# Optimization experiments

Hardware: AMD Instinct MI355X
Metric: run time of the kernel (lower is better)

The kernel has to match this reference:

```python
import jax, jax.numpy as jnp
import numpy as np

N = 2800        # real node count (before hardcoded pad)
NPAD = 3000     # module pads node dim to 3000
F_IN = 8192     # node_features
H1 = 256        # dim_h1 (GCLSTM in_channels)
H2 = 128        # GCLSTM out_channels
E = 179200      # edges (avg degree 64)


def setup_inputs() -> dict:
    key = jax.random.key(0)
    ks = jax.random.split(key, 12)
    inp = {
        "x": jax.random.normal(ks[0], (N, F_IN), jnp.float32),
        "edge_index": jax.random.randint(ks[1], (2, E), 0, N, dtype=jnp.int64),
        "edge_weight": jax.random.uniform(ks[2], (E,), jnp.float32),
        "h0": jax.random.normal(ks[3], (NPAD, H2), jnp.float32),
        "c0": jax.random.normal(ks[4], (NPAD, H2), jnp.float32),
        # fc0: node_features -> dim_h1
        "fc0_w": jax.random.normal(ks[5], (F_IN, H1), jnp.float32) / np.float32(np.sqrt(F_IN)),
        "fc0_b": jnp.zeros((H1,), jnp.float32),
        # GCLSTM gate params, stacked over gates [i, f, c, o]
        "Wx": jax.random.normal(ks[6], (4, H1, H2), jnp.float32) / np.float32(np.sqrt(H1)),
        "bg": jnp.zeros((4, H2), jnp.float32),
        # ChebConv (K=2) weights per gate: theta_0, theta_1, bias
        "cw0": jax.random.normal(ks[7], (4, H2, H2), jnp.float32) / np.float32(np.sqrt(H2)),
        "cw1": jax.random.normal(ks[8], (4, H2, H2), jnp.float32) / np.float32(np.sqrt(H2)),
        "cb": jnp.zeros((4, H2), jnp.float32),
        # final fc: 128 -> 1
        "fc_w": jax.random.normal(ks[9], (H2, 1), jnp.float32) / np.float32(np.sqrt(H2)),
        "fc_b": jnp.zeros((1,), jnp.float32),
    }
    return inp


def _cheb_scaled_laplacian(edge_index, edge_weight, num_nodes):
    # ChebConv 'sym' norm with lambda_max=2: L_hat = -D^{-1/2} A D^{-1/2}
    # (diagonal of scaled Laplacian cancels to zero with fill_value=-1 self loops)
    row, col = edge_index[0], edge_index[1]
    deg = jax.ops.segment_sum(edge_weight, row, num_segments=num_nodes)
    dinv = jnp.where(deg > 0, jax.lax.rsqrt(jnp.where(deg > 0, deg, 1.0)), 0.0)
    return -dinv[row] * edge_weight * dinv[col]  # per-edge weight of L_hat


def reference(x, edge_weight, h0, c0, fc0_w, fc0_b, Wx, bg, cw0, cw1, cb,
              fc_w, fc_b, edge_index):
    n_real = x.shape[0]
    # hardcoded zero-padding of node dim to 3000
    xp = jnp.concatenate([x, jnp.zeros((NPAD - n_real, x.shape[1]), x.dtype)], axis=0)
    z = jax.nn.relu(xp @ fc0_w + fc0_b)                       # [3000, 256]

    row, col = edge_index[0], edge_index[1]
    w_hat = _cheb_scaled_laplacian(edge_index, edge_weight, NPAD)
    # Chebyshev T1 term: L_hat @ H  (shared across all four gates)
    T1 = jax.ops.segment_sum(w_hat[:, None] * h0[row], col, num_segments=NPAD)  # [3000,128]

    # all four gate pre-activations at once: X W_x + ChebConv(H) + b
    gates = (jnp.einsum('nf,gfo->gno', z, Wx)
             + jnp.einsum('nd,gdo->gno', h0, cw0)
             + jnp.einsum('nd,gdo->gno', T1, cw1)
             + (bg + cb)[:, None, :])                          # [4, 3000, 128]

    i = jax.nn.sigmoid(gates[0])
    f = jax.nn.sigmoid(gates[1])
    t = jnp.tanh(gates[2])
    o = jax.nn.sigmoid(gates[3])
    c_new = f * c0 + i * t
    h_new = o * jnp.tanh(c_new)                                # [3000, 128]

    out = (jax.nn.relu(h_new) @ fc_w + fc_b)[:, 0]             # squeeze last dim
    out = out[:n_real]                                         # drop padding rows
    return out, h_new
```

## Files before the change

### kernel.cpp

```cpp
#include <hip/hip_runtime.h>
#include <math.h>

#define N_REAL 2800
#define NPAD   3000
#define F_IN   8192
#define H1     256
#define H2     128
#define NE     179200
#define UDIM   512
#define NGATE  512
#define MPAD   3072
#define SPLITK 8
#define KCH    (F_IN / SPLITK)
#define NHB    64
#define EPB    (NE / NHB)

typedef _Float16 half8_t __attribute__((ext_vector_type(8)));
typedef _Float16 half4_t __attribute__((ext_vector_type(4)));
typedef float    floatx4 __attribute__((ext_vector_type(4)));

__device__ __forceinline__ void async_g2l_16(const _Float16* g, _Float16* l) {
    __builtin_amdgcn_global_load_lds(
        (const __attribute__((address_space(1))) unsigned int*)g,
        (__attribute__((address_space(3))) unsigned int*)l, 16, 0, 0);
}

__global__ __launch_bounds__(256)
void prep_kernel(const float* __restrict__ w, const float* __restrict__ Wx,
                 const float* __restrict__ cw0, const float* __restrict__ cw1,
                 const float* __restrict__ bg, const float* __restrict__ cb,
                 const float* __restrict__ h0, const int* __restrict__ ei,
                 const float* __restrict__ ew,
                 _Float16* __restrict__ wTp, _Float16* __restrict__ Wcp,
                 float* __restrict__ biasv, _Float16* __restrict__ U16,
                 float* __restrict__ deg, int* __restrict__ counts,
                 int* __restrict__ cnt_pT) {
    __shared__ __align__(16) char pmem[24576];
    int b = blockIdx.x;
    int t = threadIdx.x;
    if (b < NHB) {
        float* sdeg = (float*)pmem;
        int*   scnt = (int*)(pmem + 12288);
        for (int i = t; i < 3072; i += 256) { sdeg[i] = 0.f; scnt[i] = 0; }
        __syncthreads();
        int e0 = b * EPB;
        for (int i = t; i < EPB; i += 256) {
            int e = e0 + i;
            atomicAdd(&sdeg[ei[e]], ew[e]);
            atomicAdd(&scnt[ei[NE + e]], 1);
        }
        __syncthreads();
        for (int i = t; i < 3072; i += 256) {
            atomicAdd(&deg[i], sdeg[i]);
            atomicAdd(&counts[i], scnt[i]);
            cnt_pT[i * NHB + b] = scnt[i];
        }
    } else if (b < 2112) {
        float (*tile)[33] = (float(*)[33])pmem;
        int bb = b - NHB;
        int k0 = (bb & 255) * 32;
        int n0 = (bb >> 8) * 32;
        int tx = t & 31, ty = t >> 5;
#pragma unroll
        for (int r = 0; r < 4; r++)
            tile[ty + r * 8][tx] = w[(size_t)(k0 + ty + r * 8) * H1 + n0 + tx];
        __syncthreads();
        if (t < 128) {
            int u_l = t >> 5;
            int n_l = t & 31;
            half8_t h;
#pragma unroll
            for (int j = 0; j < 8; j++) h[j] = (_Float16)tile[u_l * 8 + j][n_l];
            *(half8_t*)&wTp[(((size_t)(k0 >> 3) + u_l) * H1 + n0 + n_l) * 8] = h;
        }
    } else if (b < 3136) {
        int idx = (b - 2112) * 256 + t;
        if (idx < UDIM * NGATE) {
            int col = idx >> 9;
            int f   = idx & 511;
            int g = col >> 7, o = col & 127;
            float v;
            if (f < H1)            v = Wx[((size_t)g * H1 + f) * H2 + o];
            else if (f < H1 + H2)  v = cw0[((size_t)g * H2 + (f - H1)) * H2 + o];
            else                   v = cw1[((size_t)g * H2 + (f - H1 - H2)) * H2 + o];
            Wcp[(((size_t)(f >> 3)) * NGATE + col) * 8 + (f & 7)] = (_Float16)v;
            if (f == 0) biasv[col] = bg[col] + cb[col];
        }
    } else {
        int q = (b - 3136) * 256 + t;
        int m = q >> 5;
        int o4 = (q & 31) * 4;
        half4_t h = {};
        if (m < NPAD) {
            float4 v = *(const float4*)&h0[(size_t)m * H2 + o4];
            h[0] = (_Float16)v.x; h[1] = (_Float16)v.y; h[2] = (_Float16)v.z; h[3] = (_Float16)v.w;
        }
        *(half4_t*)&U16[(size_t)m * UDIM + H1 + o4] = h;
    }
}

__device__ __forceinline__ void stage_b1(const _Float16* __restrict__ wTp,
                                         _Float16 (*bs)[256][8], int wave, int lane, size_t kb8) {
    const _Float16* bbase = wTp + kb8 * (H1 * 8);
#pragma unroll
    for (int q = 0; q < 2; q++) {
        int u = wave * 2 + q;
#pragma unroll
        for (int rg = 0; rg < 4; rg++)
            async_g2l_16(bbase + ((size_t)u * H1 + rg * 64 + lane) * 8,
                         &bs[u][rg * 64 + lane][0]);
    }
}

__device__ __forceinline__ void put_a1(_Float16 (*as)[64][8], int arow, int aseg,
                                       const float4* A) {
    half8_t hlo, hhi;
    hlo[0] = (_Float16)A[0].x; hlo[1] = (_Float16)A[0].y; hlo[2] = (_Float16)A[0].z; hlo[3] = (_Float16)A[0].w;
    hlo[4] = (_Float16)A[1].x; hlo[5] = (_Float16)A[1].y; hlo[6] = (_Float16)A[1].z; hlo[7] = (_Float16)A[1].w;
    hhi[0] = (_Float16)A[2].x; hhi[1] = (_Float16)A[2].y; hhi[2] = (_Float16)A[2].z; hhi[3] = (_Float16)A[2].w;
    hhi[4] = (_Float16)A[3].x; hhi[5] = (_Float16)A[3].y; hhi[6] = (_Float16)A[3].z; hhi[7] = (_Float16)A[3].w;
    *(half8_t*)&as[aseg * 2][arow][0]     = hlo;
    *(half8_t*)&as[aseg * 2 + 1][arow][0] = hhi;
}

__device__ __forceinline__ void comp64(floatx4 (&acc)[4][4], _Float16 (*as)[64][8],
                                       _Float16 (*bs)[256][8], int wave, int u4, int l16) {
#pragma unroll
    for (int ks = 0; ks < 2; ks++) {
        half8_t a[4], bfr[4];
#pragma unroll
        for (int i = 0; i < 4; i++) a[i] = *(const half8_t*)&as[ks * 4 + u4][i * 16 + l16][0];
#pragma unroll
        for (int j = 0; j < 4; j++) bfr[j] = *(const half8_t*)&bs[ks * 4 + u4][wave * 64 + j * 16 + l16][0];
#pragma unroll
        for (int i = 0; i < 4; i++)
#pragma unroll
            for (int j = 0; j < 4; j++)
                acc[i][j] = __builtin_amdgcn_mfma_f32_16x16x32_f16(a[i], bfr[j], acc[i][j], 0, 0, 0);
    }
}

#define LOADA1(A, off) do { if (avalid) { \
    A[0] = *(const float4*)(agp + (off));      A[1] = *(const float4*)(agp + (off) + 4); \
    A[2] = *(const float4*)(agp + (off) + 8);  A[3] = *(const float4*)(agp + (off) + 12); } } while (0)

__global__ __launch_bounds__(256, 2)
void gemm1_fused(const float* __restrict__ x, const _Float16* __restrict__ wTp,
                 float* __restrict__ P) {
    __shared__ __align__(16) _Float16 As[2][8][64][8];
    __shared__ __align__(16) _Float16 Bs[2][8][256][8];
    const int t = threadIdx.x;
    const int wave = t >> 6, lane = t & 63;
    const int l16 = lane & 15, u4 = lane >> 4;
    const int m0 = blockIdx.x * 64;
    const int kbase = blockIdx.y * KCH;

    const int arow = t >> 2;
    const int aseg = t & 3;
    const bool avalid = (m0 + arow) < N_REAL;
    const float* agp = x + (size_t)(m0 + arow) * F_IN + kbase + aseg * 16;

    floatx4 acc[4][4] = {};
    float4 A0[4] = {}, A1[4] = {};

    LOADA1(A0, 0);
    stage_b1(wTp, Bs[0], wave, lane, (size_t)kbase >> 3);
    put_a1(As[0], arow, aseg, A0);
    LOADA1(A1, 64);
    LOADA1(A0, 128);
    __syncthreads();

    for (int q8 = 0; q8 < 8; ++q8) {
        const int k = 2 * q8;
        stage_b1(wTp, Bs[1], wave, lane, (size_t)(kbase + (k + 1) * 64) >> 3);
        put_a1(As[1], arow, aseg, A1);
        if (q8 < 7) LOADA1(A1, (k + 3) * 64);
        comp64(acc, As[0], Bs[0], wave, u4, l16);
        __syncthreads();
        if (q8 < 7) {
            stage_b1(wTp, Bs[0], wave, lane, (size_t)(kbase + (k + 2) * 64) >> 3);
            put_a1(As[0], arow, aseg, A0);
            if (q8 < 6) LOADA1(A0, (k + 4) * 64);
        }
        comp64(acc, As[1], Bs[1], wave, u4, l16);
        __syncthreads();
    }

    float* Pb = P + ((size_t)blockIdx.y * MPAD + m0) * H1;
#pragma unroll
    for (int i = 0; i < 4; i++)
#pragma unroll
        for (int j = 0; j < 4; j++) {
            int n = wave * 64 + j * 16 + l16;
#pragma unroll
            for (int r = 0; r < 4; r++)
                Pb[(size_t)(i * 16 + u4 * 4 + r) * H1 + n] = acc[i][j][r];
        }
}

__device__ __forceinline__ void zreduce_body(int zb, int t, const float* __restrict__ P,
                                             const float* __restrict__ fc0_b,
                                             _Float16* __restrict__ U16) {
    int q = zb * 256 + t;
    int m = q >> 6;
    int n4 = (q & 63) * 4;
    float s0 = 0.f, s1 = 0.f, s2 = 0.f, s3 = 0.f;
#pragma unroll
    for (int sk = 0; sk < SPLITK; sk++) {
        float4 p = *(const float4*)&P[((size_t)sk * MPAD + m) * H1 + n4];
        s0 += p.x; s1 += p.y; s2 += p.z; s3 += p.w;
    }
    float4 bb = *(const float4*)&fc0_b[n4];
    half4_t h;
    h[0] = (_Float16)fmaxf(s0 + bb.x, 0.f);
    h[1] = (_Float16)fmaxf(s1 + bb.y, 0.f);
    h[2] = (_Float16)fmaxf(s2 + bb.z, 0.f);
    h[3] = (_Float16)fmaxf(s3 + bb.w, 0.f);
    *(half4_t*)&U16[(size_t)m * UDIM + n4] = h;
}

__global__ __launch_bounds__(256)
void scatterz_kernel(const int* __restrict__ ei, const int* __restrict__ counts,
                     const float* __restrict__ deg, const int* __restrict__ cnt_pT,
                     int* __restrict__ offsets, float* __restrict__ dinv,
                     int* __restrict__ eid,
                     const float* __restrict__ P, const float* __restrict__ fc0_b,
                     _Float16* __restrict__ U16) {
    __shared__ int sb[3072];
    __shared__ int wt[4];
    int b = blockIdx.x;
    int t = threadIdx.x;
    if (b < NHB + 1) {
        int i0 = t * 12;
        int v[12]; int s = 0;
#pragma unroll
        for (int j = 0; j < 12; j++) { v[j] = counts[i0 + j]; s += v[j]; }
        int incl = s;
#pragma unroll
        for (int d = 1; d < 64; d <<= 1) {
            int n = __shfl_up(incl, d);
            if ((t & 63) >= d) incl += n;
        }
        if ((t & 63) == 63) wt[t >> 6] = incl;
        __syncthreads();
        int wbase = 0;
#pragma unroll
        for (int w = 0; w < 4; w++) wbase += (w < (t >> 6)) ? wt[w] : 0;
        int run = wbase + incl - s;
        if (b < NHB) {
#pragma unroll
            for (int j = 0; j < 12; j++) {
                const int4* cp = (const int4*)(cnt_pT + (size_t)(i0 + j) * NHB);
                int base = 0;
#pragma unroll
                for (int q4 = 0; q4 < 16; q4++) {
                    int4 v4 = cp[q4];
                    int i4 = q4 * 4;
                    base += (i4     < b ? v4.x : 0) + (i4 + 1 < b ? v4.y : 0)
                          + (i4 + 2 < b ? v4.z : 0) + (i4 + 3 < b ? v4.w : 0);
                }
                sb[i0 + j] = run + base;
                run += v[j];
            }
            __syncthreads();
            int e0 = b * EPB;
            for (int i = t; i < EPB; i += 256) {
                int e = e0 + i;
                int c = ei[NE + e];
                int p = atomicAdd(&sb[c], 1);
                eid[p] = e;
            }
        } else {
#pragma unroll
            for (int j = 0; j < 12; j++) { offsets[i0 + j] = run; run += v[j]; }
            for (int i = t; i < NPAD; i += 256) {
                float d = deg[i];
                dinv[i] = (d > 0.f) ? rsqrtf(d) : 0.f;
            }
        }
    } else {
        zreduce_body(b - NHB - 1, t, P, fc0_b, U16);
    }
}

__global__ __launch_bounds__(128)
void gather_kernel(const int* __restrict__ ei, const float* __restrict__ ew,
                   const float* __restrict__ h0, const float* __restrict__ dinv,
                   const int* __restrict__ offsets, const int* __restrict__ eid,
                   _Float16* __restrict__ U16) {
    __shared__ int   sr[128];
    __shared__ float sw[128];
    int n = blockIdx.x;
    int t = threadIdx.x;
    int beg = offsets[n], end = offsets[n + 1];
    float dc = dinv[n];
    float acc = 0.f;
    for (int base = beg; base < end; base += 128) {
        int j = base + t;
        if (j < end) {
            int e = eid[j];
            int r = ei[e];
            sr[t] = r;
            sw[t] = -dinv[r] * ew[e];
        }
        __syncthreads();
        int cnt = min(128, end - base);
        int k = 0;
        for (; k + 8 <= cnt; k += 8) {
            int   r0 = sr[k],   r1 = sr[k+1], r2 = sr[k+2], r3 = sr[k+3];
            int   r4 = sr[k+4], r5 = sr[k+5], r6 = sr[k+6], r7 = sr[k+7];
            float w0 = sw[k],   w1 = sw[k+1], w2 = sw[k+2], w3 = sw[k+3];
            float w4 = sw[k+4], w5 = sw[k+5], w6 = sw[k+6], w7 = sw[k+7];
            float v0 = h0[(size_t)r0 * H2 + t];
            float v1 = h0[(size_t)r1 * H2 + t];
            float v2 = h0[(size_t)r2 * H2 + t];
            float v3 = h0[(size_t)r3 * H2 + t];
            float v4 = h0[(size_t)r4 * H2 + t];
            float v5 = h0[(size_t)r5 * H2 + t];
            float v6 = h0[(size_t)r6 * H2 + t];
            float v7 = h0[(size_t)r7 * H2 + t];
            acc += w0 * v0 + w1 * v1 + w2 * v2 + w3 * v3
                 + w4 * v4 + w5 * v5 + w6 * v6 + w7 * v7;
        }
        for (; k < cnt; k++)
            acc += sw[k] * h0[(size_t)sr[k] * H2 + t];
        __syncthreads();
    }
    U16[(size_t)n * UDIM + H1 + H2 + t] = (_Float16)(acc * dc);
}

__global__ __launch_bounds__(256, 1)
void gemm2lstm(const _Float16* __restrict__ U16, const _Float16* __restrict__ Wcp,
               const float* __restrict__ c0, const float* __restrict__ biasv,
               const float* __restrict__ fc_w, const float* __restrict__ fc_b,
               float* __restrict__ out) {
    __shared__ __align__(16) char smem[73728];
    _Float16 (*As)[64][8]  = (_Float16(*)[64][8])smem;
    _Float16 (*Bs)[512][8] = (_Float16(*)[512][8])(smem + 8192);
    const int t = threadIdx.x;
    const int wave = t >> 6, lane = t & 63;
    const int l16 = lane & 15, u4 = lane >> 4;
    const int m0 = blockIdx.x * 64;

    floatx4 acc[4][8] = {};

    for (int kk = 0; kk < UDIM; kk += 64) {
        const _Float16* bbase = Wcp + ((size_t)(kk >> 3)) * (NGATE * 8);
#pragma unroll
        for (int q = 0; q < 2; q++) {
            int u = wave * 2 + q;
            async_g2l_16(U16 + (size_t)(m0 + lane) * UDIM + kk + u * 8, &As[u][lane][0]);
#pragma unroll
            for (int rg = 0; rg < 8; rg++)
                async_g2l_16(bbase + ((size_t)u * NGATE + rg * 64 + lane) * 8,
                             &Bs[u][rg * 64 + lane][0]);
        }
        __syncthreads();
#pragma unroll
        for (int ks = 0; ks < 2; ks++) {
            half8_t a[4], bfr[8];
#pragma unroll
            for (int i = 0; i < 4; i++) a[i] = *(const half8_t*)&As[ks * 4 + u4][i * 16 + l16][0];
#pragma unroll
            for (int j = 0; j < 8; j++) bfr[j] = *(const half8_t*)&Bs[ks * 4 + u4][wave * 128 + j * 16 + l16][0];
#pragma unroll
            for (int i = 0; i < 4; i++)
#pragma unroll
                for (int j = 0; j < 8; j++)
                    acc[i][j] = __builtin_amdgcn_mfma_f32_16x16x32_f16(a[i], bfr[j], acc[i][j], 0, 0, 0);
        }
        __syncthreads();
    }

    float* sg = (float*)smem;
#pragma unroll
    for (int h = 0; h < 2; ++h) {
#pragma unroll
        for (int ii = 0; ii < 2; ii++) {
            int i = h * 2 + ii;
#pragma unroll
            for (int j = 0; j < 8; j++)
#pragma unroll
                for (int r = 0; r < 4; r++)
                    sg[(ii * 16 + u4 * 4 + r) * 516 + wave * 128 + j * 16 + l16] = acc[i][j][r];
        }
        __syncthreads();
        int r = t >> 3;
        int og = t & 7;
        int n = m0 + h * 32 + r;
        float rsum = 0.f;
        if (n < NPAD) {
#pragma unroll
            for (int k2 = 0; k2 < 16; k2++) {
                int o = og + k2 * 8;
                float gi = sg[r * 516 + o]       + biasv[o];
                float gf = sg[r * 516 + 128 + o] + biasv[128 + o];
                float gt = sg[r * 516 + 256 + o] + biasv[256 + o];
                float go = sg[r * 516 + 384 + o] + biasv[384 + o];
                float iv = 1.f / (1.f + expf(-gi));
                float fv = 1.f / (1.f + expf(-gf));
                float tv = tanhf(gt);
                float ov = 1.f / (1.f + expf(-go));
                float c = fv * c0[(size_t)n * H2 + o] + iv * tv;
                float hh = ov * tanhf(c);
                out[N_REAL + (size_t)n * H2 + o] = hh;
                rsum += fmaxf(hh, 0.f) * fc_w[o];
            }
        }
        rsum += __shfl_down(rsum, 4);
        rsum += __shfl_down(rsum, 2);
        rsum += __shfl_down(rsum, 1);
        if ((t & 7) == 0 && n < N_REAL) out[n] = rsum + fc_b[0];
        __syncthreads();
    }
}

extern "C" void kernel_launch(void* const* d_in, const int* in_sizes, int n_in,
                              void* d_out, int out_size, void* d_ws, size_t ws_size,
                              hipStream_t stream) {
    const float* x     = (const float*)d_in[0];
    const int*   ei    = (const int*)d_in[1];
    const float* ew    = (const float*)d_in[2];
    const float* h0    = (const float*)d_in[3];
    const float* c0    = (const float*)d_in[4];
    const float* fc0_w = (const float*)d_in[5];
    const float* fc0_b = (const float*)d_in[6];
    const float* Wx    = (const float*)d_in[7];
    const float* bg    = (const float*)d_in[8];
    const float* cw0   = (const float*)d_in[9];
    const float* cw1   = (const float*)d_in[10];
    const float* cb    = (const float*)d_in[11];
    const float* fc_w  = (const float*)d_in[12];
    const float* fc_b  = (const float*)d_in[13];
    float* out = (float*)d_out;

    float* P        = (float*)d_ws;
    float* biasv    = P + (size_t)SPLITK * MPAD * H1;
    float* dinv     = biasv + NGATE;
    float* deg      = dinv + 3072;
    int*   counts   = (int*)(deg + 3072);
    int*   offs     = counts + 3072;
    int*   cnt_pT   = offs + 3072;
    int*   eid      = cnt_pT + 3072 * NHB;
    _Float16* U16 = (_Float16*)(((uintptr_t)(eid + NE) + 255) & ~(uintptr_t)255);
    _Float16* Wcp = U16 + (size_t)MPAD * UDIM;
    _Float16* wTp = Wcp + (size_t)UDIM * NGATE;

    hipMemsetAsync(deg, 0, 2 * 3072 * sizeof(float), stream);
    prep_kernel<<<3520, 256, 0, stream>>>(fc0_w, Wx, cw0, cw1, bg, cb, h0, ei, ew,
                                          wTp, Wcp, biasv, U16, deg, counts, cnt_pT);
    gemm1_fused<<<dim3(MPAD / 64, SPLITK), 256, 0, stream>>>(x, wTp, P);
    scatterz_kernel<<<NHB + 1 + 768, 256, 0, stream>>>(ei, counts, deg, cnt_pT, offs, dinv,
                                                       eid, P, fc0_b, U16);
    gather_kernel<<<NPAD, 128, 0, stream>>>(ei, ew, h0, dinv, offs, eid, U16);
    gemm2lstm<<<MPAD / 64, 256, 0, stream>>>(U16, Wcp, c0, biasv, fc_w, fc_b, out);
}
```

Before: 281.0 us.

## Double split-K factor and halve per-stage K tile in fc0 GEMM

Raises the split-K factor of the first GEMM from 8 to 16, which doubles the grid of blocks, and halves the K-step per pipeline stage from 64 to 32. The LDS buffers shrink accordingly and launch bounds are raised to allow four blocks per CU. The goal is higher occupancy and more parallel blocks for the bandwidth-bound x read. In exchange, twice as many partial results are written to P and must be reduced, and each stage has less MFMA work relative to its syncs. The reduction kernel and the P buffer must already handle SPLITK=16.

```diff
diff --git a/kernel.cpp b/kernel.cpp
--- a/kernel.cpp
+++ b/kernel.cpp
@@ -10,7 +10,7 @@
 #define UDIM   512
 #define NGATE  512
 #define MPAD   3072
-#define SPLITK 8
+#define SPLITK 16
 #define KCH    (F_IN / SPLITK)
 #define NHB    64
 #define EPB    (NE / NHB)
@@ -99,90 +99,79 @@
     }
 }
 
-__device__ __forceinline__ void stage_b1(const _Float16* __restrict__ wTp,
-                                         _Float16 (*bs)[256][8], int wave, int lane, size_t kb8) {
-    const _Float16* bbase = wTp + kb8 * (H1 * 8);
-#pragma unroll
-    for (int q = 0; q < 2; q++) {
-        int u = wave * 2 + q;
-#pragma unroll
-        for (int rg = 0; rg < 4; rg++)
-            async_g2l_16(bbase + ((size_t)u * H1 + rg * 64 + lane) * 8,
-                         &bs[u][rg * 64 + lane][0]);
-    }
-}
-
-__device__ __forceinline__ void put_a1(_Float16 (*as)[64][8], int arow, int aseg,
-                                       const float4* A) {
-    half8_t hlo, hhi;
-    hlo[0] = (_Float16)A[0].x; hlo[1] = (_Float16)A[0].y; hlo[2] = (_Float16)A[0].z; hlo[3] = (_Float16)A[0].w;
-    hlo[4] = (_Float16)A[1].x; hlo[5] = (_Float16)A[1].y; hlo[6] = (_Float16)A[1].z; hlo[7] = (_Float16)A[1].w;
-    hhi[0] = (_Float16)A[2].x; hhi[1] = (_Float16)A[2].y; hhi[2] = (_Float16)A[2].z; hhi[3] = (_Float16)A[2].w;
-    hhi[4] = (_Float16)A[3].x; hhi[5] = (_Float16)A[3].y; hhi[6] = (_Float16)A[3].z; hhi[7] = (_Float16)A[3].w;
-    *(half8_t*)&as[aseg * 2][arow][0]     = hlo;
-    *(half8_t*)&as[aseg * 2 + 1][arow][0] = hhi;
-}
-
-__device__ __forceinline__ void comp64(floatx4 (&acc)[4][4], _Float16 (*as)[64][8],
+__device__ __forceinline__ void stage_b32(const _Float16* __restrict__ wTp,
+                                          _Float16 (*bs)[256][8], int wave, int lane, size_t kb8) {
+#pragma unroll
+    for (int rg = 0; rg < 4; rg++)
+        async_g2l_16(wTp + ((kb8 + wave) * H1 + rg * 64 + lane) * 8,
+                     &bs[wave][rg * 64 + lane][0]);
+}
+
+__device__ __forceinline__ void put_a32(_Float16 (*as)[64][8], int arow, int au,
+                                        const float4* A) {
+    half8_t h;
+    h[0] = (_Float16)A[0].x; h[1] = (_Float16)A[0].y; h[2] = (_Float16)A[0].z; h[3] = (_Float16)A[0].w;
+    h[4] = (_Float16)A[1].x; h[5] = (_Float16)A[1].y; h[6] = (_Float16)A[1].z; h[7] = (_Float16)A[1].w;
+    *(half8_t*)&as[au][arow][0] = h;
+}
+
+__device__ __forceinline__ void comp32(floatx4 (&acc)[4][4], _Float16 (*as)[64][8],
                                        _Float16 (*bs)[256][8], int wave, int u4, int l16) {
-#pragma unroll
-    for (int ks = 0; ks < 2; ks++) {
-        half8_t a[4], bfr[4];
-#pragma unroll
-        for (int i = 0; i < 4; i++) a[i] = *(const half8_t*)&as[ks * 4 + u4][i * 16 + l16][0];
-#pragma unroll
-        for (int j = 0; j < 4; j++) bfr[j] = *(const half8_t*)&bs[ks * 4 + u4][wave * 64 + j * 16 + l16][0];
-#pragma unroll
-        for (int i = 0; i < 4; i++)
-#pragma unroll
-            for (int j = 0; j < 4; j++)
-                acc[i][j] = __builtin_amdgcn_mfma_f32_16x16x32_f16(a[i], bfr[j], acc[i][j], 0, 0, 0);
-    }
-}
-
-#define LOADA1(A, off) do { if (avalid) { \
-    A[0] = *(const float4*)(agp + (off));      A[1] = *(const float4*)(agp + (off) + 4); \
-    A[2] = *(const float4*)(agp + (off) + 8);  A[3] = *(const float4*)(agp + (off) + 12); } } while (0)
-
-__global__ __launch_bounds__(256, 2)
+    half8_t a[4], bfr[4];
+#pragma unroll
+    for (int i = 0; i < 4; i++) a[i] = *(const half8_t*)&as[u4][i * 16 + l16][0];
+#pragma unroll
+    for (int j = 0; j < 4; j++) bfr[j] = *(const half8_t*)&bs[u4][wave * 64 + j * 16 + l16][0];
+#pragma unroll
+    for (int i = 0; i < 4; i++)
+#pragma unroll
+        for (int j = 0; j < 4; j++)
+            acc[i][j] = __builtin_amdgcn_mfma_f32_16x16x32_f16(a[i], bfr[j], acc[i][j], 0, 0, 0);
+}
+
+#define LOADA32(A, koff) do { if (avalid) { \
+    A[0] = *(const float4*)(agp + (koff)); A[1] = *(const float4*)(agp + (koff) + 4); } } while (0)
+
+__global__ __launch_bounds__(256, 4)
 void gemm1_fused(const float* __restrict__ x, const _Float16* __restrict__ wTp,
                  float* __restrict__ P) {
-    __shared__ __align__(16) _Float16 As[2][8][64][8];
-    __shared__ __align__(16) _Float16 Bs[2][8][256][8];
+    __shared__ __align__(16) _Float16 As[2][4][64][8];
+    __shared__ __align__(16) _Float16 Bs[2][4][256][8];
     const int t = threadIdx.x;
     const int wave = t >> 6, lane = t & 63;
     const int l16 = lane & 15, u4 = lane >> 4;
     const int m0 = blockIdx.x * 64;
     const int kbase = blockIdx.y * KCH;
+    const size_t kb8 = (size_t)kbase >> 3;
 
     const int arow = t >> 2;
-    const int aseg = t & 3;
+    const int au   = t & 3;
     const bool avalid = (m0 + arow) < N_REAL;
-    const float* agp = x + (size_t)(m0 + arow) * F_IN + kbase + aseg * 16;
+    const float* agp = x + (size_t)(m0 + arow) * F_IN + kbase + au * 8;
 
     floatx4 acc[4][4] = {};
-    float4 A0[4] = {}, A1[4] = {};
-
-    LOADA1(A0, 0);
-    stage_b1(wTp, Bs[0], wave, lane, (size_t)kbase >> 3);
-    put_a1(As[0], arow, aseg, A0);
-    LOADA1(A1, 64);
-    LOADA1(A0, 128);
+    float4 A0[2] = {}, A1[2] = {};
+
+    LOADA32(A0, 0);
+    stage_b32(wTp, Bs[0], wave, lane, kb8);
+    put_a32(As[0], arow, au, A0);
+    LOADA32(A1, 32);
+    LOADA32(A0, 64);
     __syncthreads();
 
     for (int q8 = 0; q8 < 8; ++q8) {
-        const int k = 2 * q8;
-        stage_b1(wTp, Bs[1], wave, lane, (size_t)(kbase + (k + 1) * 64) >> 3);
-        put_a1(As[1], arow, aseg, A1);
-        if (q8 < 7) LOADA1(A1, (k + 3) * 64);
-        comp64(acc, As[0], Bs[0], wave, u4, l16);
+        const int s = 2 * q8;
+        stage_b32(wTp, Bs[1], wave, lane, kb8 + (size_t)(s + 1) * 4);
+        put_a32(As[1], arow, au, A1);
+        if (q8 < 7) LOADA32(A1, (s + 3) * 32);
+        comp32(acc, As[0], Bs[0], wave, u4, l16);
         __syncthreads();
         if (q8 < 7) {
-            stage_b1(wTp, Bs[0], wave, lane, (size_t)(kbase + (k + 2) * 64) >> 3);
-            put_a1(As[0], arow, aseg, A0);
-            if (q8 < 6) LOADA1(A0, (k + 4) * 64);
-        }
-        comp64(acc, As[1], Bs[1], wave, u4, l16);
+            stage_b32(wTp, Bs[0], wave, lane, kb8 + (size_t)(s + 2) * 4);
+            put_a32(As[0], arow, au, A0);
+            if (q8 < 6) LOADA32(A0, (s + 4) * 32);
+        }
+        comp32(acc, As[1], Bs[1], wave, u4, l16);
         __syncthreads();
     }
 
```

Measured after the change: 282.5 us. No clear change (+0.5%).
